# Performance work log

Hardware: AMD Instinct MI355X
Metric: run time of the kernel (lower is better)

## Reference

```python
import jax, jax.numpy as jnp
import numpy as np
import math

N_H = 16
REL_K = 16  # relative-position clamp window


def setup_inputs() -> dict:
    key = jax.random.key(0)
    ks = jax.random.split(key, 7)
    B, S, D = 8, 1024, 1024
    d_k = D // N_H
    scale = 0.02
    return {
        "x": jax.random.normal(ks[0], (B, S, D), dtype=jnp.float32),
        "W_attn": jax.random.normal(ks[1], (D, 3 * D), dtype=jnp.float32) * scale,
        "b_attn": jax.random.normal(ks[2], (3 * D,), dtype=jnp.float32) * scale,
        "W_proj": jax.random.normal(ks[3], (D, D), dtype=jnp.float32) * scale,
        "b_proj": jax.random.normal(ks[4], (D,), dtype=jnp.float32) * scale,
        "lut_k": jax.random.normal(ks[5], (2 * REL_K + 1, d_k), dtype=jnp.float32) * scale,
        "lut_v": jax.random.normal(ks[6], (2 * REL_K + 1, d_k), dtype=jnp.float32) * scale,
    }


def reference(x, W_attn, b_attn, W_proj, b_proj, lut_k, lut_v):
    B, S, D = x.shape
    d_k = D // N_H

    qkv = x @ W_attn + b_attn  # [B, S, 3D]
    q, k, v = jnp.split(qkv, 3, axis=-1)
    # [B, H, S, d_k]
    q = q.reshape(B, S, N_H, d_k).transpose(0, 2, 1, 3)
    k = k.reshape(B, S, N_H, d_k).transpose(0, 2, 1, 3)
    v = v.reshape(B, S, N_H, d_k).transpose(0, 2, 1, 3)

    i = jnp.arange(S)[:, None]
    j = jnp.arange(S)[None, :]
    rel = jnp.clip(j - i, -REL_K, REL_K) + REL_K  # [S, S] in [0, 2k]
    aij_k = lut_k[rel]  # [S, S, d_k]
    aij_v = lut_v[rel]  # [S, S, d_k]

    scores = jnp.einsum('bhid,bhjd->bhij', q, k)
    scores = scores + jnp.einsum('bhid,ijd->bhij', q, aij_k)
    scores = scores * (1.0 / math.sqrt(d_k))

    causal = j <= i  # [S, S]
    scores = jnp.where(causal[None, None, :, :], scores, -jnp.inf)
    attn = jax.nn.softmax(scores, axis=-1)  # [B, H, S, S]

    out = jnp.einsum('bhij,bhjd->bhid', attn, v)
    out = out + jnp.einsum('bhij,ijd->bhid', attn, aij_v)
    out = out.transpose(0, 2, 1, 3).reshape(B, S, D)
    return out @ W_proj + b_proj
```

## Files before the change

kernel.cpp:

```cpp
#include <hip/hip_runtime.h>
#include <hip/hip_bf16.h>
#include <math.h>

#define NH 16
#define S_LEN 1024
#define DK 64
#define D_MODEL 1024
#define HSZ 8388608

typedef __attribute__((ext_vector_type(8))) short bf16x8;
typedef __attribute__((ext_vector_type(4))) float f32x4;
typedef unsigned short USH;

#define EXPSCALE 0.1803368801111204f

__device__ __forceinline__ float fast_exp2(float x) {
    return __builtin_amdgcn_exp2f(x);
}

__device__ __forceinline__ short f2b(float x) {
    union { __hip_bfloat16 h; short s; } u;
    u.h = __float2bfloat16(x);
    return u.s;
}
__device__ __forceinline__ float b2f(USH u) {
    union { unsigned i; float f; } x;
    x.i = (unsigned)u << 16;
    return x.f;
}

__device__ __forceinline__ void gload16(const void* src, void* lds) {
    __builtin_amdgcn_global_load_lds(
        (const __attribute__((address_space(1))) void*)src,
        (__attribute__((address_space(3))) void*)lds,
        16, 0, 0);
}

__global__ __launch_bounds__(256)
void prep_kernel(const float* __restrict__ x, USH* __restrict__ xb,
                 const float* __restrict__ W_attn, USH* __restrict__ watt,
                 const float* __restrict__ W_proj, USH* __restrict__ wproj) {
    const int blk = blockIdx.x;
    const int t = threadIdx.x;
    if (blk < 4096) {
        const int i = (blk * 256 + t) * 8;
        const float4 a = *(const float4*)&x[i];
        const float4 b = *(const float4*)&x[i + 4];
        ushort4 o0, o1;
        o0.x = (USH)f2b(a.x); o0.y = (USH)f2b(a.y); o0.z = (USH)f2b(a.z); o0.w = (USH)f2b(a.w);
        o1.x = (USH)f2b(b.x); o1.y = (USH)f2b(b.y); o1.z = (USH)f2b(b.z); o1.w = (USH)f2b(b.w);
        *(ushort4*)&xb[i] = o0;
        *(ushort4*)&xb[i + 4] = o1;
        return;
    }
    __shared__ USH Ts[64][65];
    const float* in;
    USH* out;
    int R, C, r0, c0;
    if (blk < 4864) {
        const int idx = blk - 4096;
        in = W_attn; out = watt; R = 1024; C = 3072;
        c0 = (idx % 48) * 64; r0 = (idx / 48) * 64;
    } else {
        const int idx = blk - 4864;
        in = W_proj; out = wproj; R = 1024; C = 1024;
        c0 = (idx % 16) * 64; r0 = (idx / 16) * 64;
    }
    const int tr = t >> 4;
    const int tc4 = (t & 15) * 4;
    #pragma unroll
    for (int ph = 0; ph < 4; ++ph) {
        const int r = ph * 16 + tr;
        const float4 v = *(const float4*)&in[(size_t)(r0 + r) * C + c0 + tc4];
        Ts[tc4 + 0][r] = (USH)f2b(v.x);
        Ts[tc4 + 1][r] = (USH)f2b(v.y);
        Ts[tc4 + 2][r] = (USH)f2b(v.z);
        Ts[tc4 + 3][r] = (USH)f2b(v.w);
    }
    __syncthreads();
    #pragma unroll
    for (int ph = 0; ph < 4; ++ph) {
        const int cc = ph * 16 + tr;
        ushort4 o;
        o.x = Ts[cc][tc4 + 0]; o.y = Ts[cc][tc4 + 1];
        o.z = Ts[cc][tc4 + 2]; o.w = Ts[cc][tc4 + 3];
        *(ushort4*)&out[(size_t)(c0 + cc) * R + r0 + tc4] = o;
    }
}

__global__ __launch_bounds__(256)
void vtransp_kernel(const USH* __restrict__ in, USH* __restrict__ out) {
    __shared__ USH T[64][72];
    const int bh = blockIdx.x >> 4;
    const int s0 = (blockIdx.x & 15) * 64;
    const int r = threadIdx.x >> 4;
    const int c4 = (threadIdx.x & 15) * 4;
    #pragma unroll
    for (int ph = 0; ph < 4; ++ph) {
        const int row = ph * 16 + r;
        const ushort4 v = *(const ushort4*)
            &in[((size_t)bh * S_LEN + s0 + row) * DK + c4];
        T[row][c4 + 0] = v.x; T[row][c4 + 1] = v.y;
        T[row][c4 + 2] = v.z; T[row][c4 + 3] = v.w;
    }
    __syncthreads();
    #pragma unroll
    for (int ph = 0; ph < 4; ++ph) {
        const int d = ph * 16 + r;
        ushort4 o;
        o.x = T[c4 + 0][d]; o.y = T[c4 + 1][d];
        o.z = T[c4 + 2][d]; o.w = T[c4 + 3][d];
        *(ushort4*)&out[(size_t)bh * (S_LEN * DK) + (size_t)d * S_LEN + s0 + c4] = o;
    }
}

__global__ __launch_bounds__(512)
void qkv_gemm_kernel(const USH* __restrict__ A, const USH* __restrict__ Bt,
                     const float* __restrict__ bias,
                     USH* __restrict__ Cq, USH* __restrict__ Ck,
                     USH* __restrict__ Cv) {
    __shared__ __align__(16) USH lds[3 * 16384];
    const int t = threadIdx.x;
    const int w = t >> 6, lane = t & 63, g = lane >> 4, c = lane & 15;
    const int wm = w >> 2, wn = w & 3;
    const int bid = blockIdx.x;
    const int swz = (bid & 7) * 48 + (bid >> 3);
    const int bn0 = (swz % 12) * 256;
    const int bm0 = (swz / 12) * 256;

    auto stage = [&](int kt, int slot) {
        const int k0 = kt * 32;
        USH* base = lds + slot * 16384;
        #pragma unroll
        for (int q = 0; q < 2; ++q) {
            const int o = t * 16 + q * 8192;
            const int row = o >> 6;
            const int chunk = (o >> 4) & 3;
            const int sc = (chunk ^ (row & 3)) * 8;
            gload16(A + (size_t)(bm0 + row) * 1024 + k0 + sc, (char*)base + o);
            gload16(Bt + (size_t)(bn0 + row) * 1024 + k0 + sc,
                    (char*)(base + 8192) + o);
        }
    };

    unsigned aoff[8], boff[4];
    #pragma unroll
    for (int i = 0; i < 8; ++i) {
        const int row = wm * 128 + i * 16 + c;
        aoff[i] = (unsigned)(row * 64) + (((unsigned)(g ^ (row & 3))) << 4);
    }
    #pragma unroll
    for (int j = 0; j < 4; ++j) {
        const int row = wn * 64 + j * 16 + c;
        boff[j] = 16384u + (unsigned)(row * 64) + (((unsigned)(g ^ (row & 3))) << 4);
    }

    f32x4 acc[8][4];
    #pragma unroll
    for (int i = 0; i < 8; ++i)
        #pragma unroll
        for (int j = 0; j < 4; ++j) acc[i][j] = (f32x4)0.f;

    stage(0, 0);
    stage(1, 1);

    int cur = 0;
    for (int kt = 0; kt < 32; ++kt) {
        if (kt < 31) asm volatile("s_waitcnt vmcnt(4)" ::: "memory");
        else         asm volatile("s_waitcnt vmcnt(0)" ::: "memory");
        __builtin_amdgcn_s_barrier();

        const int slot2 = (cur + 2 >= 3) ? cur - 1 : cur + 2;
        if (kt + 2 < 32)
            stage(kt + 2, slot2);

        const char* sb = (const char*)lds + cur * 32768;
        bf16x8 af[8], bfr[4];
        #pragma unroll
        for (int i = 0; i < 8; ++i) af[i] = *(const bf16x8*)(sb + aoff[i]);
        #pragma unroll
        for (int j = 0; j < 4; ++j) bfr[j] = *(const bf16x8*)(sb + boff[j]);

        __builtin_amdgcn_s_setprio(1);
        #pragma unroll
        for (int i = 0; i < 8; ++i)
            #pragma unroll
            for (int j = 0; j < 4; ++j)
                acc[i][j] = __builtin_amdgcn_mfma_f32_16x16x32_bf16(
                    af[i], bfr[j], acc[i][j], 0, 0, 0);
        __builtin_amdgcn_s_setprio(0);

        cur = (cur + 1 == 3) ? 0 : cur + 1;
    }

    #pragma unroll
    for (int i = 0; i < 8; ++i) {
        #pragma unroll
        for (int reg = 0; reg < 4; ++reg) {
            const int m = bm0 + wm * 128 + i * 16 + g * 4 + reg;
            const int b = m >> 10, s = m & 1023;
            #pragma unroll
            for (int j = 0; j < 4; ++j) {
                const int n = bn0 + wn * 64 + j * 16 + c;
                const float v = acc[i][j][reg] + bias[n];
                const int which = n >> 10;
                const int h = (n & 1023) >> 6, d = n & 63;
                const size_t idx = (((size_t)(b * NH + h)) * S_LEN + s) * DK + d;
                if (which == 0)      Cq[idx] = (USH)f2b(v);
                else if (which == 1) Ck[idx] = (USH)f2b(v);
                else                 Cv[idx] = (USH)f2b(v);
            }
        }
    }
}

__global__ __launch_bounds__(256)
void proj_gemm_kernel(const USH* __restrict__ A, const USH* __restrict__ Bt,
                      const float* __restrict__ bias, float* __restrict__ Cf,
                      int M, int N, int K) {
    __shared__ __align__(16) USH As[128 * 32];
    __shared__ __align__(16) USH Bs[128 * 32];
    const int t = threadIdx.x;
    const int w = t >> 6, lane = t & 63, g = lane >> 4, c = lane & 15;
    const int wm = w >> 1, wn = w & 1;
    const int bm0 = blockIdx.y * 128, bn0 = blockIdx.x * 128;

    const int sk = ((t & 3) ^ ((t >> 3) & 3)) * 8;
    const USH* pa0 = A + (size_t)(bm0 + (t >> 2)) * K + sk;
    const USH* pa1 = pa0 + (size_t)64 * K;
    const USH* pb0 = Bt + (size_t)(bn0 + (t >> 2)) * K + sk;
    const USH* pb1 = pb0 + (size_t)64 * K;
    USH* ldsA0 = &As[(t & ~63) * 8];
    USH* ldsA1 = ldsA0 + 2048;
    USH* ldsB0 = &Bs[(t & ~63) * 8];
    USH* ldsB1 = ldsB0 + 2048;

    unsigned aoff[4], boff[4];
    #pragma unroll
    for (int i = 0; i < 4; ++i) {
        const int r = wm * 64 + i * 16 + c;
        aoff[i] = ((unsigned)(r * 64 + g * 16)) ^ ((((unsigned)r >> 1) & 3) << 4);
        const int n = wn * 64 + i * 16 + c;
        boff[i] = ((unsigned)(n * 64 + g * 16)) ^ ((((unsigned)n >> 1) & 3) << 4);
    }

    f32x4 acc[4][4];
    #pragma unroll
    for (int i = 0; i < 4; ++i)
        #pragma unroll
        for (int j = 0; j < 4; ++j) acc[i][j] = (f32x4)0.f;

    for (int k0 = 0; k0 < K; k0 += 32) {
        gload16(pa0 + k0, ldsA0);
        gload16(pa1 + k0, ldsA1);
        gload16(pb0 + k0, ldsB0);
        gload16(pb1 + k0, ldsB1);
        __syncthreads();

        bf16x8 af[4], bfr[4];
        #pragma unroll
        for (int i = 0; i < 4; ++i) af[i] = *(const bf16x8*)((const char*)As + aoff[i]);
        #pragma unroll
        for (int j = 0; j < 4; ++j) bfr[j] = *(const bf16x8*)((const char*)Bs + boff[j]);
        #pragma unroll
        for (int i = 0; i < 4; ++i)
            #pragma unroll
            for (int j = 0; j < 4; ++j)
                acc[i][j] = __builtin_amdgcn_mfma_f32_16x16x32_bf16(
                    af[i], bfr[j], acc[i][j], 0, 0, 0);
        __syncthreads();
    }

    #pragma unroll
    for (int i = 0; i < 4; ++i) {
        #pragma unroll
        for (int reg = 0; reg < 4; ++reg) {
            const int m = bm0 + wm * 64 + i * 16 + g * 4 + reg;
            #pragma unroll
            for (int j = 0; j < 4; ++j) {
                const int n = bn0 + wn * 64 + j * 16 + c;
                Cf[(size_t)m * N + n] = acc[i][j][reg] + bias[n];
            }
        }
    }
}

__global__ __launch_bounds__(512, 4)
void attn_mfma_kernel(const USH* __restrict__ qb,
                      const USH* __restrict__ kbuf,
                      const USH* __restrict__ vtg,
                      const float* __restrict__ lut_k,
                      const float* __restrict__ lut_v,
                      USH* __restrict__ ao) {
    const int bid = blockIdx.x;
    const int logical = (bid & 7) * 128 + (bid >> 3);
    const int ib = 7 - (logical & 7);
    const int bh = logical >> 3;
    const int b = bh >> 4, h = bh & 15;
    const int i0 = ib * 128;
    const int t = threadIdx.x;
    const int w = t >> 6;
    const int lane = t & 63;
    const int g = lane >> 4;
    const int c = lane & 15;

    __shared__ __align__(16) char smem[76928];
    char* pb     = smem + 49152;
    char* qsb    = smem + 49152;
    char* lutkb  = smem + 8192;
    USH* qrelb   = (USH*)(smem + 65536);
    USH* lvfb    = (USH*)(smem + 70656);
    USH* tapssb  = (USH*)(smem + 72832);

    const USH* qp  = qb   + (size_t)bh * (S_LEN * DK);
    const USH* kp  = kbuf + (size_t)bh * (S_LEN * DK);
    const USH* vtp = vtg  + (size_t)bh * (S_LEN * DK);

    auto stage = [&](int j0, int slot) {
        const int o = t * 16;
        const int row = o >> 7;
        const int chunk = (o >> 4) & 7;
        const int sc = (chunk ^ (row & 7)) * 8;
        gload16(kp + (size_t)(j0 + row) * DK + sc, smem + slot * 8192 + o);
        gload16(vtp + (size_t)row * S_LEN + j0 + sc, smem + 24576 + slot * 8192 + o);
    };

    stage(0, 0);
    for (int f = t; f < 2048; f += 512) {
        const int row = f >> 4, c4 = (f & 15) * 4;
        unsigned byte = ((unsigned)(row * 128 + c4 * 2)) ^ (((unsigned)row & 7) << 4);
        *(ushort4*)(qsb + byte) = *(const ushort4*)&qp[(size_t)(i0 + row) * DK + c4];
    }
    for (int e = t; e < 32 * 64; e += 512) {
        const int row = e >> 6, d = e & 63;
        const USH v = (row < 17) ? (USH)f2b(lut_k[row * 64 + d]) : (USH)0;
        unsigned byte = ((unsigned)(row * 128 + d * 2)) ^ (((unsigned)row & 7) << 4);
        *(USH*)(lutkb + byte) = v;
    }
    for (int e = t; e < 17 * 64; e += 512)
        lvfb[e] = (USH)f2b(lut_v[e]);
    __syncthreads();

    bf16x8 qa[2];
    {
        const int row = w * 16 + c;
        #pragma unroll
        for (int kh = 0; kh < 2; ++kh) {
            unsigned byte = ((unsigned)(row * 128 + kh * 64 + g * 16))
                          ^ (((unsigned)row & 7) << 4);
            qa[kh] = *(const bf16x8*)(qsb + byte);
        }
    }

    {
        f32x4 qr[2];
        qr[0] = (f32x4)0.f; qr[1] = (f32x4)0.f;
        #pragma unroll
        for (int sub2 = 0; sub2 < 2; ++sub2) {
            const int tap = sub2 * 16 + c;
            #pragma unroll
            for (int kh = 0; kh < 2; ++kh) {
                unsigned byte = ((unsigned)(tap * 128 + kh * 64 + g * 16))
                              ^ (((unsigned)tap & 7) << 4);
                bf16x8 lb = *(const bf16x8*)(lutkb + byte);
                qr[sub2] = __builtin_amdgcn_mfma_f32_16x16x32_bf16(
                    qa[kh], lb, qr[sub2], 0, 0, 0);
            }
        }
        #pragma unroll
        for (int sub2 = 0; sub2 < 2; ++sub2) {
            const int tap = sub2 * 16 + c;
            if (tap < 17) {
                #pragma unroll
                for (int r = 0; r < 4; ++r)
                    qrelb[(w * 16 + g * 4 + r) * 20 + tap] = (USH)f2b(qr[sub2][r]);
            }
        }
    }
    float qrel0s[4];
    #pragma unroll
    for (int r = 0; r < 4; ++r)
        qrel0s[r] = b2f(qrelb[(w * 16 + g * 4 + r) * 20]) * EXPSCALE;

    __syncthreads();

    const int NT = 2 * ib + 2;
    if (1 < NT) stage(64, 1);

    f32x4 acc[4];
    #pragma unroll
    for (int dt = 0; dt < 4; ++dt) acc[dt] = (f32x4)0.f;
    float l_r[4];
    #pragma unroll
    for (int r = 0; r < 4; ++r) l_r[r] = 0.f;

    const int wrow0 = i0 + w * 16;
    int cur = 0;
    for (int tile = 0; tile < NT; ++tile) {
        const int nxt2 = tile + 2;
        const int slot2 = (cur + 2 >= 3) ? cur - 1 : cur + 2;
        if (nxt2 < NT)
            stage(nxt2 << 6, slot2);

        if (tile * 64 > wrow0 + 15) {
            if (nxt2 < NT) asm volatile("s_waitcnt vmcnt(2)" ::: "memory");
            else           asm volatile("s_waitcnt vmcnt(0)" ::: "memory");
            __builtin_amdgcn_s_barrier();
            cur = (cur + 1 == 3) ? 0 : cur + 1;
            continue;
        }

        const char* ktb = smem + cur * 8192;
        const char* vtb = smem + 24576 + cur * 8192;

        float p[4][4];
        __builtin_amdgcn_s_setprio(1);
        f32x4 s[4];
        #pragma unroll
        for (int sub = 0; sub < 4; ++sub) {
            s[sub] = (f32x4)0.f;
            const int krow = sub * 16 + c;
            #pragma unroll
            for (int kh = 0; kh < 2; ++kh) {
                unsigned byte = ((unsigned)krow << 7) + ((unsigned)kh << 6) + ((unsigned)g << 4);
                byte ^= (unsigned)(krow & 7) << 4;
                bf16x8 kb = *(const bf16x8*)(ktb + byte);
                s[sub] = __builtin_amdgcn_mfma_f32_16x16x32_bf16(qa[kh], kb, s[sub], 0, 0, 0);
            }
        }
        __builtin_amdgcn_s_setprio(0);

        if (tile * 64 + 79 <= wrow0) {
            #pragma unroll
            for (int sub = 0; sub < 4; ++sub)
                #pragma unroll
                for (int r = 0; r < 4; ++r)
                    p[sub][r] = fast_exp2(s[sub][r] * EXPSCALE + qrel0s[r]);
        } else {
            #pragma unroll
            for (int sub = 0; sub < 4; ++sub) {
                const int dbase = tile * 64 + (sub * 16 + c) - i0 - (w * 16 + g * 4);
                #pragma unroll
                for (int r = 0; r < 4; ++r) {
                    const int dj = dbase - r;
                    int t17 = dj + 16;
                    t17 = t17 < 0 ? 0 : (t17 > 16 ? 16 : t17);
                    const int il = w * 16 + g * 4 + r;
                    float pv = fast_exp2((s[sub][r] + b2f(qrelb[il * 20 + t17])) * EXPSCALE);
                    if (dj > 0) pv = 0.f;
                    p[sub][r] = pv;
                    if (dj >= -15 && dj <= 0)
                        tapssb[il * 16 + dj + 15] = (USH)f2b(pv);
                }
            }
        }

        #pragma unroll
        for (int r = 0; r < 4; ++r)
            l_r[r] += (p[0][r] + p[1][r]) + (p[2][r] + p[3][r]);

        char* pw = pb + w * 2048;
        #pragma unroll
        for (int sub = 0; sub < 4; ++sub)
            #pragma unroll
            for (int r = 0; r < 4; ++r) {
                const int row = g * 4 + r;
                unsigned byte = ((unsigned)row << 7) + (((unsigned)(sub * 16 + c)) << 1);
                byte ^= (unsigned)(row & 7) << 4;
                *(short*)(pw + byte) = f2b(p[sub][r]);
            }

        bf16x8 pa[2];
        #pragma unroll
        for (int jh = 0; jh < 2; ++jh) {
            unsigned byte = ((unsigned)c << 7) + ((unsigned)jh << 6) + ((unsigned)g << 4);
            byte ^= (unsigned)(c & 7) << 4;
            pa[jh] = *(const bf16x8*)(pw + byte);
        }
        __builtin_amdgcn_s_setprio(1);
        #pragma unroll
        for (int dt = 0; dt < 4; ++dt) {
            const int d = dt * 16 + c;
            #pragma unroll
            for (int jh = 0; jh < 2; ++jh) {
                unsigned byte = ((unsigned)d << 7) + ((unsigned)jh << 6) + ((unsigned)g << 4);
                byte ^= (unsigned)(d & 7) << 4;
                bf16x8 vb = *(const bf16x8*)(vtb + byte);
                acc[dt] = __builtin_amdgcn_mfma_f32_16x16x32_bf16(pa[jh], vb, acc[dt], 0, 0, 0);
            }
        }
        __builtin_amdgcn_s_setprio(0);

        if (nxt2 < NT) asm volatile("s_waitcnt vmcnt(2)" ::: "memory");
        else           asm volatile("s_waitcnt vmcnt(0)" ::: "memory");
        __builtin_amdgcn_s_barrier();
        cur = (cur + 1 == 3) ? 0 : cur + 1;
    }

    const int rbase = w * 16 + g * 4;
    #pragma unroll
    for (int r = 0; r < 4; ++r) {
        float lsum = l_r[r];
        #pragma unroll
        for (int msk = 1; msk < 16; msk <<= 1)
            lsum += __shfl_xor(lsum, msk);
        const int il = rbase + r;
        float c0 = lsum;
        float tp[16];
        #pragma unroll
        for (int tap = 0; tap < 16; ++tap) {
            const int jg = i0 + il + tap - 15;
            const float pv = (jg >= 0) ? b2f(tapssb[il * 16 + tap]) : 0.f;
            tp[tap] = pv;
            c0 -= pv;
        }
        const float invl = 1.f / lsum;
        #pragma unroll
        for (int dt = 0; dt < 4; ++dt) {
            const int d = dt * 16 + c;
            float o = acc[dt][r] + c0 * b2f(lvfb[d]);
            #pragma unroll
            for (int tap = 0; tap < 16; ++tap)
                o += tp[tap] * b2f(lvfb[(tap + 1) * 64 + d]);
            o *= invl;
            ao[((size_t)b * S_LEN + (i0 + il)) * D_MODEL + h * DK + d] = (USH)f2b(o);
        }
    }
}

extern "C" void kernel_launch(void* const* d_in, const int* in_sizes, int n_in,
                              void* d_out, int out_size, void* d_ws, size_t ws_size,
                              hipStream_t stream) {
    const float* x      = (const float*)d_in[0];
    const float* W_attn = (const float*)d_in[1];
    const float* b_attn = (const float*)d_in[2];
    const float* W_proj = (const float*)d_in[3];
    const float* b_proj = (const float*)d_in[4];
    const float* lut_k  = (const float*)d_in[5];
    const float* lut_v  = (const float*)d_in[6];
    float* out = (float*)d_out;

    USH* qb    = (USH*)d_ws;
    USH* kb    = qb + HSZ;
    USH* vb    = kb + HSZ;
    USH* vtg   = vb + HSZ;
    USH* aob   = vtg + HSZ;
    USH* xb    = aob + HSZ;
    USH* watt  = xb + HSZ;
    USH* wproj = watt + 3145728;

    prep_kernel<<<5120, 256, 0, stream>>>(x, xb, W_attn, watt, W_proj, wproj);

    qkv_gemm_kernel<<<384, 512, 0, stream>>>(xb, watt, b_attn, qb, kb, vb);

    vtransp_kernel<<<2048, 256, 0, stream>>>(vb, vtg);

    attn_mfma_kernel<<<1024, 512, 0, stream>>>(qb, kb, vtg, lut_k, lut_v, aob);

    proj_gemm_kernel<<<dim3(1024 / 128, 8192 / 128), 256, 0, stream>>>(
        aob, wproj, b_proj, out, 8192, 1024, 1024);
}
```

Measured before the change: 199.2 us.

## Fuse V transpose into QKV GEMM epilogue and share 256x128 GEMM for projection

Replaces the 256x256 QKV GEMM plus separate V-transpose kernel with a templated 256x128-tile GEMM whose epilogue writes V already transposed, staged through LDS. This removes one kernel launch and a full round trip of V through global memory. The output projection now uses the same triple-buffered, swizzled 256x128 kernel instead of the simpler single-buffered 128x128 one. Smaller tiles double the QKV block count, which helps occupancy and wave balance but lowers per-block data reuse.

```diff
diff --git a/kernel.cpp b/kernel.cpp
--- a/kernel.cpp
+++ b/kernel.cpp
@@ -88,76 +88,51 @@
     }
 }
 
-__global__ __launch_bounds__(256)
-void vtransp_kernel(const USH* __restrict__ in, USH* __restrict__ out) {
-    __shared__ USH T[64][72];
-    const int bh = blockIdx.x >> 4;
-    const int s0 = (blockIdx.x & 15) * 64;
-    const int r = threadIdx.x >> 4;
-    const int c4 = (threadIdx.x & 15) * 4;
-    #pragma unroll
-    for (int ph = 0; ph < 4; ++ph) {
-        const int row = ph * 16 + r;
-        const ushort4 v = *(const ushort4*)
-            &in[((size_t)bh * S_LEN + s0 + row) * DK + c4];
-        T[row][c4 + 0] = v.x; T[row][c4 + 1] = v.y;
-        T[row][c4 + 2] = v.z; T[row][c4 + 3] = v.w;
-    }
-    __syncthreads();
-    #pragma unroll
-    for (int ph = 0; ph < 4; ++ph) {
-        const int d = ph * 16 + r;
-        ushort4 o;
-        o.x = T[c4 + 0][d]; o.y = T[c4 + 1][d];
-        o.z = T[c4 + 2][d]; o.w = T[c4 + 3][d];
-        *(ushort4*)&out[(size_t)bh * (S_LEN * DK) + (size_t)d * S_LEN + s0 + c4] = o;
-    }
-}
-
+template<int QKV>
 __global__ __launch_bounds__(512)
-void qkv_gemm_kernel(const USH* __restrict__ A, const USH* __restrict__ Bt,
-                     const float* __restrict__ bias,
-                     USH* __restrict__ Cq, USH* __restrict__ Ck,
-                     USH* __restrict__ Cv) {
-    __shared__ __align__(16) USH lds[3 * 16384];
+void gemm256_kernel(const USH* __restrict__ A, const USH* __restrict__ Bt,
+                    const float* __restrict__ bias,
+                    float* __restrict__ Cf, USH* __restrict__ Cq,
+                    USH* __restrict__ Ck, USH* __restrict__ Cvt,
+                    int N, int NTILN) {
+    __shared__ __align__(16) USH lds[36864];
     const int t = threadIdx.x;
     const int w = t >> 6, lane = t & 63, g = lane >> 4, c = lane & 15;
-    const int wm = w >> 2, wn = w & 3;
+    const int wm = w >> 1, wn = w & 1;
+    const int nwg = NTILN * 32;
     const int bid = blockIdx.x;
-    const int swz = (bid & 7) * 48 + (bid >> 3);
-    const int bn0 = (swz % 12) * 256;
-    const int bm0 = (swz / 12) * 256;
+    const int swz = (bid & 7) * (nwg >> 3) + (bid >> 3);
+    const int bn0 = (swz % NTILN) * 128;
+    const int bm0 = (swz / NTILN) * 256;
 
     auto stage = [&](int kt, int slot) {
         const int k0 = kt * 32;
-        USH* base = lds + slot * 16384;
+        char* base = (char*)lds + slot * 24576;
         #pragma unroll
         for (int q = 0; q < 2; ++q) {
             const int o = t * 16 + q * 8192;
             const int row = o >> 6;
-            const int chunk = (o >> 4) & 3;
-            const int sc = (chunk ^ (row & 3)) * 8;
-            gload16(A + (size_t)(bm0 + row) * 1024 + k0 + sc, (char*)base + o);
-            gload16(Bt + (size_t)(bn0 + row) * 1024 + k0 + sc,
-                    (char*)(base + 8192) + o);
-        }
+            const int sc = (((o >> 4) & 3) ^ (row & 3)) * 8;
+            gload16(A + (size_t)(bm0 + row) * 1024 + k0 + sc, base + o);
+        }
+        const int o = t * 16;
+        const int row = o >> 6;
+        const int sc = (((o >> 4) & 3) ^ (row & 3)) * 8;
+        gload16(Bt + (size_t)(bn0 + row) * 1024 + k0 + sc, base + 16384 + o);
     };
 
-    unsigned aoff[8], boff[4];
-    #pragma unroll
-    for (int i = 0; i < 8; ++i) {
-        const int row = wm * 128 + i * 16 + c;
+    unsigned aoff[4], boff[4];
+    #pragma unroll
+    for (int i = 0; i < 4; ++i) {
+        const int row = wm * 64 + i * 16 + c;
         aoff[i] = (unsigned)(row * 64) + (((unsigned)(g ^ (row & 3))) << 4);
-    }
-    #pragma unroll
-    for (int j = 0; j < 4; ++j) {
-        const int row = wn * 64 + j * 16 + c;
-        boff[j] = 16384u + (unsigned)(row * 64) + (((unsigned)(g ^ (row & 3))) << 4);
-    }
-
-    f32x4 acc[8][4];
-    #pragma unroll
-    for (int i = 0; i < 8; ++i)
+        const int rn = wn * 64 + i * 16 + c;
+        boff[i] = 16384u + (unsigned)(rn * 64) + (((unsigned)(g ^ (rn & 3))) << 4);
+    }
+
+    f32x4 acc[4][4];
+    #pragma unroll
+    for (int i = 0; i < 4; ++i)
         #pragma unroll
         for (int j = 0; j < 4; ++j) acc[i][j] = (f32x4)0.f;
 
@@ -166,7 +141,7 @@
 
     int cur = 0;
     for (int kt = 0; kt < 32; ++kt) {
-        if (kt < 31) asm volatile("s_waitcnt vmcnt(4)" ::: "memory");
+        if (kt < 31) asm volatile("s_waitcnt vmcnt(3)" ::: "memory");
         else         asm volatile("s_waitcnt vmcnt(0)" ::: "memory");
         __builtin_amdgcn_s_barrier();
 
@@ -174,16 +149,16 @@
         if (kt + 2 < 32)
             stage(kt + 2, slot2);
 
-        const char* sb = (const char*)lds + cur * 32768;
-        bf16x8 af[8], bfr[4];
-        #pragma unroll
-        for (int i = 0; i < 8; ++i) af[i] = *(const bf16x8*)(sb + aoff[i]);
+        const char* sb = (const char*)lds + cur * 24576;
+        bf16x8 af[4], bfr[4];
+        #pragma unroll
+        for (int i = 0; i < 4; ++i) af[i] = *(const bf16x8*)(sb + aoff[i]);
         #pragma unroll
         for (int j = 0; j < 4; ++j) bfr[j] = *(const bf16x8*)(sb + boff[j]);
 
         __builtin_amdgcn_s_setprio(1);
         #pragma unroll
-        for (int i = 0; i < 8; ++i)
+        for (int i = 0; i < 4; ++i)
             #pragma unroll
             for (int j = 0; j < 4; ++j)
                 acc[i][j] = __builtin_amdgcn_mfma_f32_16x16x32_bf16(
@@ -193,93 +168,73 @@
         cur = (cur + 1 == 3) ? 0 : cur + 1;
     }
 
-    #pragma unroll
-    for (int i = 0; i < 8; ++i) {
-        #pragma unroll
-        for (int reg = 0; reg < 4; ++reg) {
-            const int m = bm0 + wm * 128 + i * 16 + g * 4 + reg;
-            const int b = m >> 10, s = m & 1023;
-            #pragma unroll
-            for (int j = 0; j < 4; ++j) {
-                const int n = bn0 + wn * 64 + j * 16 + c;
-                const float v = acc[i][j][reg] + bias[n];
-                const int which = n >> 10;
-                const int h = (n & 1023) >> 6, d = n & 63;
-                const size_t idx = (((size_t)(b * NH + h)) * S_LEN + s) * DK + d;
-                if (which == 0)      Cq[idx] = (USH)f2b(v);
-                else if (which == 1) Ck[idx] = (USH)f2b(v);
-                else                 Cv[idx] = (USH)f2b(v);
-            }
-        }
-    }
-}
-
-__global__ __launch_bounds__(256)
-void proj_gemm_kernel(const USH* __restrict__ A, const USH* __restrict__ Bt,
-                      const float* __restrict__ bias, float* __restrict__ Cf,
-                      int M, int N, int K) {
-    __shared__ __align__(16) USH As[128 * 32];
-    __shared__ __align__(16) USH Bs[128 * 32];
-    const int t = threadIdx.x;
-    const int w = t >> 6, lane = t & 63, g = lane >> 4, c = lane & 15;
-    const int wm = w >> 1, wn = w & 1;
-    const int bm0 = blockIdx.y * 128, bn0 = blockIdx.x * 128;
-
-    const int sk = ((t & 3) ^ ((t >> 3) & 3)) * 8;
-    const USH* pa0 = A + (size_t)(bm0 + (t >> 2)) * K + sk;
-    const USH* pa1 = pa0 + (size_t)64 * K;
-    const USH* pb0 = Bt + (size_t)(bn0 + (t >> 2)) * K + sk;
-    const USH* pb1 = pb0 + (size_t)64 * K;
-    USH* ldsA0 = &As[(t & ~63) * 8];
-    USH* ldsA1 = ldsA0 + 2048;
-    USH* ldsB0 = &Bs[(t & ~63) * 8];
-    USH* ldsB1 = ldsB0 + 2048;
-
-    unsigned aoff[4], boff[4];
-    #pragma unroll
-    for (int i = 0; i < 4; ++i) {
-        const int r = wm * 64 + i * 16 + c;
-        aoff[i] = ((unsigned)(r * 64 + g * 16)) ^ ((((unsigned)r >> 1) & 3) << 4);
-        const int n = wn * 64 + i * 16 + c;
-        boff[i] = ((unsigned)(n * 64 + g * 16)) ^ ((((unsigned)n >> 1) & 3) << 4);
-    }
-
-    f32x4 acc[4][4];
-    #pragma unroll
-    for (int i = 0; i < 4; ++i)
-        #pragma unroll
-        for (int j = 0; j < 4; ++j) acc[i][j] = (f32x4)0.f;
-
-    for (int k0 = 0; k0 < K; k0 += 32) {
-        gload16(pa0 + k0, ldsA0);
-        gload16(pa1 + k0, ldsA1);
-        gload16(pb0 + k0, ldsB0);
-        gload16(pb1 + k0, ldsB1);
-        __syncthreads();
-
-        bf16x8 af[4], bfr[4];
-        #pragma unroll
-        for (int i = 0; i < 4; ++i) af[i] = *(const bf16x8*)((const char*)As + aoff[i]);
-        #pragma unroll
-        for (int j = 0; j < 4; ++j) bfr[j] = *(const bf16x8*)((const char*)Bs + boff[j]);
-        #pragma unroll
-        for (int i = 0; i < 4; ++i)
-            #pragma unroll
-            for (int j = 0; j < 4; ++j)
-                acc[i][j] = __builtin_amdgcn_mfma_f32_16x16x32_bf16(
-                    af[i], bfr[j], acc[i][j], 0, 0, 0);
-        __syncthreads();
-    }
-
-    #pragma unroll
-    for (int i = 0; i < 4; ++i) {
-        #pragma unroll
-        for (int reg = 0; reg < 4; ++reg) {
-            const int m = bm0 + wm * 64 + i * 16 + g * 4 + reg;
-            #pragma unroll
-            for (int j = 0; j < 4; ++j) {
-                const int n = bn0 + wn * 64 + j * 16 + c;
-                Cf[(size_t)m * N + n] = acc[i][j][reg] + bias[n];
+    if (QKV) {
+        if (bn0 < 2048) {
+            #pragma unroll
+            for (int i = 0; i < 4; ++i) {
+                #pragma unroll
+                for (int reg = 0; reg < 4; ++reg) {
+                    const int m = bm0 + wm * 64 + i * 16 + g * 4 + reg;
+                    const int b = m >> 10, s = m & 1023;
+                    #pragma unroll
+                    for (int j = 0; j < 4; ++j) {
+                        const int n = bn0 + wn * 64 + j * 16 + c;
+                        const float v = acc[i][j][reg] + bias[n];
+                        const int which = n >> 10;
+                        const int h = (n & 1023) >> 6, d = n & 63;
+                        const size_t idx = (((size_t)(b * NH + h)) * S_LEN + s) * DK + d;
+                        if (which == 0) Cq[idx] = (USH)f2b(v);
+                        else            Ck[idx] = (USH)f2b(v);
+                    }
+                }
+            }
+        } else {
+            __syncthreads();
+            #pragma unroll
+            for (int i = 0; i < 4; ++i) {
+                const int m_local = wm * 64 + i * 16 + g * 4;
+                #pragma unroll
+                for (int j = 0; j < 4; ++j) {
+                    const int n_local = wn * 64 + j * 16 + c;
+                    const int n = bn0 + n_local;
+                    ushort4 pk;
+                    pk.x = (USH)f2b(acc[i][j][0] + bias[n]);
+                    pk.y = (USH)f2b(acc[i][j][1] + bias[n]);
+                    pk.z = (USH)f2b(acc[i][j][2] + bias[n]);
+                    pk.w = (USH)f2b(acc[i][j][3] + bias[n]);
+                    unsigned byte = ((unsigned)(n_local * 512 + m_local * 2))
+                                  ^ (((unsigned)n_local & 7) << 4);
+                    *(ushort4*)((char*)lds + byte) = pk;
+                }
+            }
+            __syncthreads();
+            const int b = bm0 >> 10, s0 = bm0 & 1023;
+            const int h0 = (bn0 & 1023) >> 6;
+            #pragma unroll
+            for (int e = 0; e < 8; ++e) {
+                const int task = e * 512 + t;
+                const int n_local = task >> 5;
+                const int chunk = task & 31;
+                unsigned byte = ((unsigned)(n_local * 512 + chunk * 16))
+                              ^ (((unsigned)n_local & 7) << 4);
+                bf16x8 v = *(const bf16x8*)((char*)lds + byte);
+                const int h = h0 + (n_local >> 6);
+                const int d = n_local & 63;
+                *(bf16x8*)&Cvt[(((size_t)(b * NH + h)) * DK + d) * S_LEN
+                               + s0 + chunk * 8] = v;
+            }
+        }
+    } else {
+        #pragma unroll
+        for (int i = 0; i < 4; ++i) {
+            #pragma unroll
+            for (int reg = 0; reg < 4; ++reg) {
+                const int m = bm0 + wm * 64 + i * 16 + g * 4 + reg;
+                #pragma unroll
+                for (int j = 0; j < 4; ++j) {
+                    const int n = bn0 + wn * 64 + j * 16 + c;
+                    Cf[(size_t)m * N + n] = acc[i][j][reg] + bias[n];
+                }
             }
         }
     }
@@ -551,12 +506,11 @@
 
     prep_kernel<<<5120, 256, 0, stream>>>(x, xb, W_attn, watt, W_proj, wproj);
 
-    qkv_gemm_kernel<<<384, 512, 0, stream>>>(xb, watt, b_attn, qb, kb, vb);
-
-    vtransp_kernel<<<2048, 256, 0, stream>>>(vb, vtg);
+    gemm256_kernel<1><<<768, 512, 0, stream>>>(
+        xb, watt, b_attn, nullptr, qb, kb, vtg, 3072, 24);
 
     attn_mfma_kernel<<<1024, 512, 0, stream>>>(qb, kb, vtg, lut_k, lut_v, aob);
 
-    proj_gemm_kernel<<<dim3(1024 / 128, 8192 / 128), 256, 0, stream>>>(
-        aob, wproj, b_proj, out, 8192, 1024, 1024);
-}
+    gemm256_kernel<0><<<256, 512, 0, stream>>>(
+        aob, wproj, b_proj, out, nullptr, nullptr, nullptr, 1024, 8);
+}
```

After: 179.0 us. 1.11x faster.
